# Performance work log

Measured on AMD Instinct MI355X. Metric: run time of the kernel, lower is better.

Reference implementation:

```python
import jax, jax.numpy as jnp
import numpy as np
from functools import partial

N_NODES = 100000
N_EDGES = 3200000
F_IN, H1, H2, C_OUT = 128, 64, 32, 2


def setup_inputs() -> dict:
    key = jax.random.key(0)
    ks = jax.random.split(key, 8)
    x = jax.random.normal(ks[0], (N_NODES, F_IN), dtype=jnp.float32)
    edge_index = jax.random.randint(ks[1], (2, N_EDGES), 0, N_NODES, dtype=jnp.int64)
    def glorot(k, fan_in, fan_out):
        s = jnp.sqrt(6.0 / (fan_in + fan_out))
        return jax.random.uniform(k, (fan_in, fan_out), jnp.float32, -s, s)
    return {
        "x": x,
        "edge_index": edge_index,
        "W1": glorot(ks[2], F_IN, H1), "b1": jnp.zeros((H1,), jnp.float32),
        "W2": glorot(ks[3], H1, H2),   "b2": jnp.zeros((H2,), jnp.float32),
        "W3": glorot(ks[4], H2, C_OUT), "b3": jnp.zeros((C_OUT,), jnp.float32),
    }


def _gcn_norm(edge_index, num_nodes):
    # add self-loops, compute symmetric normalization D^{-1/2} (A+I) D^{-1/2}
    loop = jnp.arange(num_nodes, dtype=edge_index.dtype)
    src = jnp.concatenate([edge_index[0], loop])
    dst = jnp.concatenate([edge_index[1], loop])
    deg = jax.ops.segment_sum(jnp.ones_like(dst, dtype=jnp.float32), dst,
                              num_segments=num_nodes)
    dinv = jax.lax.rsqrt(deg)  # deg >= 1 because of self-loops
    norm = dinv[src] * dinv[dst]  # [E + N]
    return src, dst, norm


def _gcn_conv(x, W, b, src, dst, norm, num_nodes):
    # PyG GCNConv: linear transform, then normalized scatter-aggregate, then bias
    xw = x @ W                                   # [N, F_out]
    msg = xw[src] * norm[:, None]                # [E+N, F_out] gather + scale
    out = jax.ops.segment_sum(msg, dst, num_segments=num_nodes)
    return out + b


def reference(x, edge_index, W1, b1, W2, b2, W3, b3):
    n = x.shape[0]
    src, dst, norm = _gcn_norm(edge_index, n)
    h = jax.nn.relu(_gcn_conv(x, W1, b1, src, dst, norm, n))
    # dropout is identity in eval mode
    h = jax.nn.relu(_gcn_conv(h, W2, b2, src, dst, norm, n))
    h = _gcn_conv(h, W3, b3, src, dst, norm, n)
    return jax.nn.log_softmax(h, axis=1)
```

## Files before the change

### kernel.cpp

```cpp
#include <hip/hip_runtime.h>
#include <hip/hip_bf16.h>
#include <math.h>

constexpr int N = 100000;
constexpr int E = 3200000;
constexpr int FIN = 128, H1 = 64, H2 = 32, COUT = 2;

constexpr int BUK_SHIFT = 6;
constexpr int BUK_NODES = 64;
constexpr int NBUK = (N + BUK_NODES - 1) / BUK_NODES;
constexpr int CAP = 2560;
constexpr int SEG_SHIFT = 14;
constexpr int NSEG = 7;
constexpr int KEYS = BUK_NODES * NSEG;
constexpr int RP_STR = BUK_NODES + 1;

constexpr int MS_TPB = 1024;
constexpr int MS_EPT = 24;
constexpr int CHUNK = MS_TPB * MS_EPT;
constexpr int MS_WGS = (E + CHUNK - 1) / CHUNK;

typedef float f32x4 __attribute__((ext_vector_type(4)));
typedef short bf16x8 __attribute__((ext_vector_type(8)));
typedef short s16x4 __attribute__((ext_vector_type(4)));

__global__ void k_initcur(int* __restrict__ gcursor) {
    int i = blockIdx.x * blockDim.x + threadIdx.x;
    if (i < NBUK) gcursor[i] = i * CAP;
}

__global__ __launch_bounds__(MS_TPB)
void k_mslice(const int* __restrict__ src, const int* __restrict__ dst,
              int* __restrict__ gcursor, unsigned* __restrict__ ebuf) {
    __shared__ int cnt[NBUK];
    __shared__ int base[NBUK];
    const int t = threadIdx.x;
    for (int i = t; i < NBUK; i += MS_TPB) cnt[i] = 0;
    __syncthreads();
    const int e0 = blockIdx.x * CHUNK;

    int rb[MS_EPT];
    unsigned rv[MS_EPT];
#pragma unroll
    for (int j = 0; j < MS_EPT; ++j) {
        int e = e0 + j * MS_TPB + t;
        if (e < E) {
            int d = dst[e];
            int b = d >> BUK_SHIFT;
            rb[j] = b;
            rv[j] = (unsigned)src[e] | ((unsigned)(d & (BUK_NODES - 1)) << 17);
            atomicAdd(&cnt[b], 1);
        } else {
            rb[j] = -1; rv[j] = 0;
        }
    }
    __syncthreads();
    for (int i = t; i < NBUK; i += MS_TPB) {
        int c = cnt[i];
        base[i] = c ? atomicAdd(&gcursor[i], c) : 0;
    }
    __syncthreads();
    for (int i = t; i < NBUK; i += MS_TPB) cnt[i] = 0;
    __syncthreads();
#pragma unroll
    for (int j = 0; j < MS_EPT; ++j) {
        int b = rb[j];
        if (b >= 0) {
            int r = atomicAdd(&cnt[b], 1);
            int p = base[b] + r;
            if (p < (b + 1) * CAP) ebuf[p] = rv[j];
        }
    }
}

__global__ __launch_bounds__(256)
void k_build(const int* __restrict__ gcursor, unsigned* __restrict__ ebuf,
             int* __restrict__ rp, float* __restrict__ dinv) {
    __shared__ unsigned ent[CAP];
    __shared__ int cnt[512];
    __shared__ int sa[512];
    __shared__ int sb[512];
    __shared__ int cur[512];
    const int b = blockIdx.x;
    const int t = threadIdx.x;
    int fill = gcursor[b] - b * CAP;
    if (fill > CAP) fill = CAP;
    const int gbase = b * CAP;

    cnt[t] = 0; cnt[t + 256] = 0;
    __syncthreads();
    for (int j = t; j < fill; j += 256) {
        unsigned v = ebuf[gbase + j];
        ent[j] = v;
        int key = (int)(v >> 17) * NSEG + (int)((v & 0x1FFFFu) >> SEG_SHIFT);
        atomicAdd(&cnt[key], 1);
    }
    __syncthreads();
    sa[t] = cnt[t]; sa[t + 256] = cnt[t + 256];
    __syncthreads();
    int* pin = sa; int* pout = sb;
    for (int off = 1; off < 512; off <<= 1) {
        pout[t]       = pin[t]       + ((t >= off)       ? pin[t - off]       : 0);
        pout[t + 256] = pin[t + 256] + ((t + 256 >= off) ? pin[t + 256 - off] : 0);
        __syncthreads();
        int* tmp = pin; pin = pout; pout = tmp;
    }
    {
        int ex0 = pin[t] - cnt[t];
        int ex1 = pin[t + 256] - cnt[t + 256];
        cur[t] = gbase + ex0;
        cur[t + 256] = gbase + ex1;
        if (t < KEYS && (t % NSEG) == 0)
            rp[b * RP_STR + t / NSEG] = gbase + ex0;
        int k2 = t + 256;
        if (k2 < KEYS && (k2 % NSEG) == 0)
            rp[b * RP_STR + k2 / NSEG] = gbase + ex1;
        if (t == 0) rp[b * RP_STR + BUK_NODES] = gbase + fill;
    }
    if (t < BUK_NODES) {
        int deg = 0;
#pragma unroll
        for (int s = 0; s < NSEG; ++s) deg += cnt[t * NSEG + s];
        int node = (b << BUK_SHIFT) + t;
        if (node < N) dinv[node] = rsqrtf((float)deg + 1.0f);
    }
    __syncthreads();
    for (int j = t; j < fill; j += 256) {
        unsigned v = ent[j];
        int key = (int)(v >> 17) * NSEG + (int)((v & 0x1FFFFu) >> SEG_SHIFT);
        int p = atomicAdd(&cur[key], 1);
        ebuf[p] = v & 0x1FFFFu;
    }
}

template<int FI, int FO>
__global__ __launch_bounds__(256)
void k_gemm_mfma(const float* __restrict__ h, const float* __restrict__ Wg,
                 const float* __restrict__ dinv, __hip_bfloat16* __restrict__ y) {
    constexpr int KH  = (FI > 64) ? 64 : FI;
    constexpr int NPH = FI / KH;
    constexpr int KP  = KH + 8;
    constexpr int NCT = FO / 16;

    __shared__ short xh[64 * KP];
    __shared__ short xl[64 * KP];
    __shared__ short wh[FO * KP];
    __shared__ short wl[FO * KP];

    const int tid = threadIdx.x;
    const int w   = tid >> 6;
    const int l   = tid & 63;
    const int lm  = l & 15;
    const int lg  = l >> 4;
    const int row0 = blockIdx.x * 64;

    auto cvt_hi = [](float f) -> short {
        __hip_bfloat16 b = __float2bfloat16(f);
        return *reinterpret_cast<short*>(&b);
    };
    auto bf2f = [](short s) -> float {
        return __uint_as_float(((unsigned)(unsigned short)s) << 16);
    };

    f32x4 acc[NCT];
#pragma unroll
    for (int ct = 0; ct < NCT; ++ct) acc[ct] = f32x4{0.f, 0.f, 0.f, 0.f};

    for (int ph = 0; ph < NPH; ++ph) {
        if (ph) __syncthreads();
        for (int idx = tid; idx < 64 * KH / 4; idx += 256) {
            int r  = idx / (KH / 4);
            int k4 = idx % (KH / 4);
            int row = row0 + r;
            float4 v = make_float4(0.f, 0.f, 0.f, 0.f);
            if (row < N) v = *(const float4*)(h + (size_t)row * FI + ph * KH + 4 * k4);
            float vv[4] = {v.x, v.y, v.z, v.w};
            s16x4 ph4, pl4;
#pragma unroll
            for (int i = 0; i < 4; ++i) {
                short hi = cvt_hi(vv[i]);
                ph4[i] = hi;
                pl4[i] = cvt_hi(vv[i] - bf2f(hi));
            }
            *(s16x4*)&xh[r * KP + 4 * k4] = ph4;
            *(s16x4*)&xl[r * KP + 4 * k4] = pl4;
        }
        for (int idx = tid; idx < KH * FO; idx += 256) {
            int k = idx / FO;
            int c = idx % FO;
            float wv = Wg[(size_t)(ph * KH + k) * FO + c];
            short hi = cvt_hi(wv);
            wh[c * KP + k] = hi;
            wl[c * KP + k] = cvt_hi(wv - bf2f(hi));
        }
        __syncthreads();

#pragma unroll
        for (int k0 = 0; k0 < KH; k0 += 32) {
            const int ka = (16 * w + lm) * KP + k0 + 8 * lg;
            bf16x8 ah = *(const bf16x8*)&xh[ka];
            bf16x8 al = *(const bf16x8*)&xl[ka];
#pragma unroll
            for (int ct = 0; ct < NCT; ++ct) {
                const int kb = (16 * ct + lm) * KP + k0 + 8 * lg;
                bf16x8 bh = *(const bf16x8*)&wh[kb];
                bf16x8 bl = *(const bf16x8*)&wl[kb];
                acc[ct] = __builtin_amdgcn_mfma_f32_16x16x32_bf16(ah, bh, acc[ct], 0, 0, 0);
                acc[ct] = __builtin_amdgcn_mfma_f32_16x16x32_bf16(ah, bl, acc[ct], 0, 0, 0);
                acc[ct] = __builtin_amdgcn_mfma_f32_16x16x32_bf16(al, bh, acc[ct], 0, 0, 0);
            }
        }
    }

    float di[4];
#pragma unroll
    for (int i = 0; i < 4; ++i) {
        int row = row0 + 16 * w + 4 * lg + i;
        di[i] = (row < N) ? dinv[row] : 0.f;
    }
#pragma unroll
    for (int ct = 0; ct < NCT; ++ct) {
#pragma unroll
        for (int i = 0; i < 4; ++i) {
            int row = row0 + 16 * w + 4 * lg + i;
            if (row < N)
                y[(size_t)row * FO + 16 * ct + lm] = __float2bfloat16(di[i] * acc[ct][i]);
        }
    }
}

template<int FI, int FO, int ROWS>
__global__ __launch_bounds__(FO * ROWS)
void k_gemm_scale(const float* __restrict__ h, const float* __restrict__ W,
                  const float* __restrict__ dinv, float* __restrict__ y) {
    __shared__ float xs[ROWS][FI];
    const int j = threadIdx.x;
    const int r = threadIdx.y;
    const int row0 = blockIdx.x * ROWS;
    const int tid = r * FO + j;
    constexpr int NT = FO * ROWS;
    for (int t = tid; t < ROWS * FI; t += NT) {
        int rr = t / FI, kk = t % FI;
        int row = row0 + rr;
        xs[rr][kk] = (row < N) ? h[(size_t)row * FI + kk] : 0.0f;
    }
    __syncthreads();
    const int row = row0 + r;
    if (row >= N) return;
    float acc = 0.0f;
#pragma unroll
    for (int k = 0; k < FI; ++k)
        acc = fmaf(xs[r][k], W[k * FO + j], acc);
    y[(size_t)row * FO + j] = dinv[row] * acc;
}

template<int F, bool RELU>
__global__ __launch_bounds__(256)
void k_agg_v(const int* __restrict__ rp, const unsigned* __restrict__ csr,
             const __hip_bfloat16* __restrict__ y, const float* __restrict__ dinv,
             const float* __restrict__ b, float* __restrict__ out) {
    constexpr int LPN = F / 8;
    constexpr int NPB = 256 / LPN;
    const int fp = threadIdx.x;
    const int n = blockIdx.x * NPB + threadIdx.y;
    if (n >= N) return;
    const uint4* yq = (const uint4*)y;

    float acc[8];
    auto unpk = [](unsigned w, float& lo, float& hi) {
        lo = __uint_as_float(w << 16);
        hi = __uint_as_float(w & 0xffff0000u);
    };
    auto accum = [&](uint4 v) {
        float l0, h0, l1, h1, l2, h2, l3, h3;
        unpk(v.x, l0, h0); unpk(v.y, l1, h1);
        unpk(v.z, l2, h2); unpk(v.w, l3, h3);
        acc[0] += l0; acc[1] += h0; acc[2] += l1; acc[3] += h1;
        acc[4] += l2; acc[5] += h2; acc[6] += l3; acc[7] += h3;
    };

    {
        uint4 v = yq[(size_t)n * LPN + fp];
        float l0, h0, l1, h1, l2, h2, l3, h3;
        unpk(v.x, l0, h0); unpk(v.y, l1, h1);
        unpk(v.z, l2, h2); unpk(v.w, l3, h3);
        acc[0] = l0; acc[1] = h0; acc[2] = l1; acc[3] = h1;
        acc[4] = l2; acc[5] = h2; acc[6] = l3; acc[7] = h3;
    }

    const int rb = (n >> BUK_SHIFT) * RP_STR + (n & (BUK_NODES - 1));
    int j = rp[rb];
    const int j1 = rp[rb + 1];
    for (; j + 8 <= j1; j += 8) {
        int s0 = (int)csr[j],     s1 = (int)csr[j + 1], s2 = (int)csr[j + 2], s3 = (int)csr[j + 3];
        int s4 = (int)csr[j + 4], s5 = (int)csr[j + 5], s6 = (int)csr[j + 6], s7 = (int)csr[j + 7];
        uint4 v0 = yq[(size_t)s0 * LPN + fp], v1 = yq[(size_t)s1 * LPN + fp];
        uint4 v2 = yq[(size_t)s2 * LPN + fp], v3 = yq[(size_t)s3 * LPN + fp];
        uint4 v4 = yq[(size_t)s4 * LPN + fp], v5 = yq[(size_t)s5 * LPN + fp];
        uint4 v6 = yq[(size_t)s6 * LPN + fp], v7 = yq[(size_t)s7 * LPN + fp];
        accum(v0); accum(v1); accum(v2); accum(v3);
        accum(v4); accum(v5); accum(v6); accum(v7);
    }
    for (; j < j1; ++j) {
        uint4 v = yq[(size_t)(int)csr[j] * LPN + fp];
        accum(v);
    }

    const float di = dinv[n];
    float4 o0, o1;
    o0.x = fmaf(di, acc[0], b[8 * fp + 0]);
    o0.y = fmaf(di, acc[1], b[8 * fp + 1]);
    o0.z = fmaf(di, acc[2], b[8 * fp + 2]);
    o0.w = fmaf(di, acc[3], b[8 * fp + 3]);
    o1.x = fmaf(di, acc[4], b[8 * fp + 4]);
    o1.y = fmaf(di, acc[5], b[8 * fp + 5]);
    o1.z = fmaf(di, acc[6], b[8 * fp + 6]);
    o1.w = fmaf(di, acc[7], b[8 * fp + 7]);
    if (RELU) {
        o0.x = fmaxf(o0.x, 0.f); o0.y = fmaxf(o0.y, 0.f);
        o0.z = fmaxf(o0.z, 0.f); o0.w = fmaxf(o0.w, 0.f);
        o1.x = fmaxf(o1.x, 0.f); o1.y = fmaxf(o1.y, 0.f);
        o1.z = fmaxf(o1.z, 0.f); o1.w = fmaxf(o1.w, 0.f);
    }
    float* op = out + (size_t)n * F + 8 * fp;
    *(float4*)op = o0;
    *(float4*)(op + 4) = o1;
}

__global__ __launch_bounds__(256)
void k_final(const int* __restrict__ rp, const unsigned* __restrict__ csr,
             const float* __restrict__ y, const float* __restrict__ dinv,
             const float* __restrict__ bias, float* __restrict__ out) {
    const int c = threadIdx.x;
    const int n = blockIdx.x * 128 + threadIdx.y;
    float z = 0.0f;
    if (n < N) {
        const int rb = (n >> BUK_SHIFT) * RP_STR + (n & (BUK_NODES - 1));
        int j = rp[rb];
        const int j1 = rp[rb + 1];
        float acc = y[2 * n + c];
        for (; j + 4 <= j1; j += 4) {
            int s0 = (int)csr[j], s1 = (int)csr[j + 1], s2 = (int)csr[j + 2], s3 = (int)csr[j + 3];
            float a0 = y[2 * s0 + c], a1 = y[2 * s1 + c];
            float a2 = y[2 * s2 + c], a3 = y[2 * s3 + c];
            acc += (a0 + a1) + (a2 + a3);
        }
        for (; j < j1; ++j) acc += y[2 * (int)csr[j] + c];
        z = fmaf(dinv[n], acc, bias[c]);
    }
    float zo = __shfl_xor(z, 1);
    if (n < N) {
        float m = fmaxf(z, zo);
        float lse = m + logf(expf(z - m) + expf(zo - m));
        out[2 * n + c] = z - lse;
    }
}

extern "C" void kernel_launch(void* const* d_in, const int* in_sizes, int n_in,
                              void* d_out, int out_size, void* d_ws, size_t ws_size,
                              hipStream_t stream) {
    const float* x   = (const float*)d_in[0];
    const int*   ei  = (const int*)d_in[1];
    const float* W1  = (const float*)d_in[2];
    const float* b1  = (const float*)d_in[3];
    const float* W2  = (const float*)d_in[4];
    const float* b2  = (const float*)d_in[5];
    const float* W3  = (const float*)d_in[6];
    const float* b3  = (const float*)d_in[7];
    float* out = (float*)d_out;

    const int* src = ei;
    const int* dst = ei + E;

    char* p = (char*)d_ws;
    float*    dinv    = (float*)p;    p += (size_t)N * 4;
    int*      gcursor = (int*)p;      p += (size_t)NBUK * 4;
    int*      rp      = (int*)p;      p += (size_t)NBUK * RP_STR * 4;
    unsigned* ebuf    = (unsigned*)p; p += (size_t)NBUK * CAP * 4;
    char*     bufA    = p;            p += (size_t)N * 64 * 4;
    char*     bufB    = p;            p += (size_t)N * 64 * 4;

    __hip_bfloat16* y1 = (__hip_bfloat16*)bufA;
    float*          h1 = (float*)bufB;
    __hip_bfloat16* y2 = (__hip_bfloat16*)bufA;
    float*          h2 = (float*)(bufA + (size_t)N * H2 * 2);
    float*          y3 = (float*)bufB;

    k_initcur<<<(NBUK + 255) / 256, 256, 0, stream>>>(gcursor);
    k_mslice <<<MS_WGS, MS_TPB, 0, stream>>>(src, dst, gcursor, ebuf);
    k_build  <<<NBUK, 256, 0, stream>>>(gcursor, ebuf, rp, dinv);

    k_gemm_mfma<FIN, H1><<<(N + 63) / 64, 256, 0, stream>>>(x, W1, dinv, y1);
    k_agg_v<H1, true><<<(N + 31) / 32, dim3(8, 32), 0, stream>>>(rp, ebuf, y1, dinv, b1, h1);

    k_gemm_mfma<H1, H2><<<(N + 63) / 64, 256, 0, stream>>>(h1, W2, dinv, y2);
    k_agg_v<H2, true><<<(N + 63) / 64, dim3(4, 64), 0, stream>>>(rp, ebuf, y2, dinv, b2, h2);

    k_gemm_scale<H2, COUT, 128><<<(N + 127) / 128, dim3(COUT, 128), 0, stream>>>(h2, W3, dinv, y3);
    k_final<<<(N + 127) / 128, dim3(2, 128), 0, stream>>>(rp, ebuf, y3, dinv, b3, out);
}
```

Baseline: 369.0 us.

## Split feature dim into 16-wide slices for cache-resident neighbor aggregation

The GEMM now writes its bf16 output slice-major ([F/16][N][16]). Aggregation runs as one launch per 16-feature slice, so each pass gathers from a 3.2 MB table that is more likely to stay in L2 or the last-level cache. Index reads and output writes use nontemporal hints so they don't evict the gathered table. In exchange the CSR indices are re-read once per slice, there are more kernel launches, and each gathered row is a 32-byte access instead of a full 128-byte row.

```diff
diff --git a/kernel.cpp b/kernel.cpp
--- a/kernel.cpp
+++ b/kernel.cpp
@@ -224,7 +224,7 @@
         for (int i = 0; i < 4; ++i) {
             int row = row0 + 16 * w + 4 * lg + i;
             if (row < N)
-                y[(size_t)row * FO + 16 * ct + lm] = __float2bfloat16(di[i] * acc[ct][i]);
+                y[((size_t)ct * N + row) * 16 + lm] = __float2bfloat16(di[i] * acc[ct][i]);
         }
     }
 }
@@ -256,21 +256,26 @@
 
 template<int F, bool RELU>
 __global__ __launch_bounds__(256)
-void k_agg_v(const int* __restrict__ rp, const unsigned* __restrict__ csr,
-             const __hip_bfloat16* __restrict__ y, const float* __restrict__ dinv,
-             const float* __restrict__ b, float* __restrict__ out) {
-    constexpr int LPN = F / 8;
-    constexpr int NPB = 256 / LPN;
+void k_agg_slice(int ps, const int* __restrict__ rp, const unsigned* __restrict__ csr,
+                 const __hip_bfloat16* __restrict__ y, const float* __restrict__ dinv,
+                 const float* __restrict__ b, float* __restrict__ out) {
     const int fp = threadIdx.x;
-    const int n = blockIdx.x * NPB + threadIdx.y;
+    const int n  = blockIdx.x * 128 + threadIdx.y;
     if (n >= N) return;
     const uint4* yq = (const uint4*)y;
-
-    float acc[8];
+    const size_t sb = (size_t)ps * N * 2 + fp;
+
     auto unpk = [](unsigned w, float& lo, float& hi) {
         lo = __uint_as_float(w << 16);
         hi = __uint_as_float(w & 0xffff0000u);
     };
+
+    float acc[8];
+    {
+        uint4 v = yq[sb + (size_t)n * 2];
+        unpk(v.x, acc[0], acc[1]); unpk(v.y, acc[2], acc[3]);
+        unpk(v.z, acc[4], acc[5]); unpk(v.w, acc[6], acc[7]);
+    }
     auto accum = [&](uint4 v) {
         float l0, h0, l1, h1, l2, h2, l3, h3;
         unpk(v.x, l0, h0); unpk(v.y, l1, h1);
@@ -279,52 +284,50 @@
         acc[4] += l2; acc[5] += h2; acc[6] += l3; acc[7] += h3;
     };
 
-    {
-        uint4 v = yq[(size_t)n * LPN + fp];
-        float l0, h0, l1, h1, l2, h2, l3, h3;
-        unpk(v.x, l0, h0); unpk(v.y, l1, h1);
-        unpk(v.z, l2, h2); unpk(v.w, l3, h3);
-        acc[0] = l0; acc[1] = h0; acc[2] = l1; acc[3] = h1;
-        acc[4] = l2; acc[5] = h2; acc[6] = l3; acc[7] = h3;
-    }
-
     const int rb = (n >> BUK_SHIFT) * RP_STR + (n & (BUK_NODES - 1));
     int j = rp[rb];
     const int j1 = rp[rb + 1];
     for (; j + 8 <= j1; j += 8) {
-        int s0 = (int)csr[j],     s1 = (int)csr[j + 1], s2 = (int)csr[j + 2], s3 = (int)csr[j + 3];
-        int s4 = (int)csr[j + 4], s5 = (int)csr[j + 5], s6 = (int)csr[j + 6], s7 = (int)csr[j + 7];
-        uint4 v0 = yq[(size_t)s0 * LPN + fp], v1 = yq[(size_t)s1 * LPN + fp];
-        uint4 v2 = yq[(size_t)s2 * LPN + fp], v3 = yq[(size_t)s3 * LPN + fp];
-        uint4 v4 = yq[(size_t)s4 * LPN + fp], v5 = yq[(size_t)s5 * LPN + fp];
-        uint4 v6 = yq[(size_t)s6 * LPN + fp], v7 = yq[(size_t)s7 * LPN + fp];
+        int s0 = (int)__builtin_nontemporal_load(&csr[j]);
+        int s1 = (int)__builtin_nontemporal_load(&csr[j + 1]);
+        int s2 = (int)__builtin_nontemporal_load(&csr[j + 2]);
+        int s3 = (int)__builtin_nontemporal_load(&csr[j + 3]);
+        int s4 = (int)__builtin_nontemporal_load(&csr[j + 4]);
+        int s5 = (int)__builtin_nontemporal_load(&csr[j + 5]);
+        int s6 = (int)__builtin_nontemporal_load(&csr[j + 6]);
+        int s7 = (int)__builtin_nontemporal_load(&csr[j + 7]);
+        uint4 v0 = yq[sb + (size_t)s0 * 2], v1 = yq[sb + (size_t)s1 * 2];
+        uint4 v2 = yq[sb + (size_t)s2 * 2], v3 = yq[sb + (size_t)s3 * 2];
+        uint4 v4 = yq[sb + (size_t)s4 * 2], v5 = yq[sb + (size_t)s5 * 2];
+        uint4 v6 = yq[sb + (size_t)s6 * 2], v7 = yq[sb + (size_t)s7 * 2];
         accum(v0); accum(v1); accum(v2); accum(v3);
         accum(v4); accum(v5); accum(v6); accum(v7);
     }
     for (; j < j1; ++j) {
-        uint4 v = yq[(size_t)(int)csr[j] * LPN + fp];
-        accum(v);
+        int s = (int)__builtin_nontemporal_load(&csr[j]);
+        accum(yq[sb + (size_t)s * 2]);
     }
 
     const float di = dinv[n];
-    float4 o0, o1;
-    o0.x = fmaf(di, acc[0], b[8 * fp + 0]);
-    o0.y = fmaf(di, acc[1], b[8 * fp + 1]);
-    o0.z = fmaf(di, acc[2], b[8 * fp + 2]);
-    o0.w = fmaf(di, acc[3], b[8 * fp + 3]);
-    o1.x = fmaf(di, acc[4], b[8 * fp + 4]);
-    o1.y = fmaf(di, acc[5], b[8 * fp + 5]);
-    o1.z = fmaf(di, acc[6], b[8 * fp + 6]);
-    o1.w = fmaf(di, acc[7], b[8 * fp + 7]);
+    const float* bp = b + ps * 16 + 8 * fp;
+    f32x4 o0, o1;
+    o0.x = fmaf(di, acc[0], bp[0]);
+    o0.y = fmaf(di, acc[1], bp[1]);
+    o0.z = fmaf(di, acc[2], bp[2]);
+    o0.w = fmaf(di, acc[3], bp[3]);
+    o1.x = fmaf(di, acc[4], bp[4]);
+    o1.y = fmaf(di, acc[5], bp[5]);
+    o1.z = fmaf(di, acc[6], bp[6]);
+    o1.w = fmaf(di, acc[7], bp[7]);
     if (RELU) {
         o0.x = fmaxf(o0.x, 0.f); o0.y = fmaxf(o0.y, 0.f);
         o0.z = fmaxf(o0.z, 0.f); o0.w = fmaxf(o0.w, 0.f);
         o1.x = fmaxf(o1.x, 0.f); o1.y = fmaxf(o1.y, 0.f);
         o1.z = fmaxf(o1.z, 0.f); o1.w = fmaxf(o1.w, 0.f);
     }
-    float* op = out + (size_t)n * F + 8 * fp;
-    *(float4*)op = o0;
-    *(float4*)(op + 4) = o1;
+    float* op = out + (size_t)n * F + ps * 16 + 8 * fp;
+    __builtin_nontemporal_store(o0, (f32x4*)op);
+    __builtin_nontemporal_store(o1, (f32x4*)(op + 4));
 }
 
 __global__ __launch_bounds__(256)
@@ -390,11 +393,15 @@
     k_mslice <<<MS_WGS, MS_TPB, 0, stream>>>(src, dst, gcursor, ebuf);
     k_build  <<<NBUK, 256, 0, stream>>>(gcursor, ebuf, rp, dinv);
 
+    const int AGG_GRID = (N + 127) / 128;
+
     k_gemm_mfma<FIN, H1><<<(N + 63) / 64, 256, 0, stream>>>(x, W1, dinv, y1);
-    k_agg_v<H1, true><<<(N + 31) / 32, dim3(8, 32), 0, stream>>>(rp, ebuf, y1, dinv, b1, h1);
+    for (int ps = 0; ps < H1 / 16; ++ps)
+        k_agg_slice<H1, true><<<AGG_GRID, dim3(2, 128), 0, stream>>>(ps, rp, ebuf, y1, dinv, b1, h1);
 
     k_gemm_mfma<H1, H2><<<(N + 63) / 64, 256, 0, stream>>>(h1, W2, dinv, y2);
-    k_agg_v<H2, true><<<(N + 63) / 64, dim3(4, 64), 0, stream>>>(rp, ebuf, y2, dinv, b2, h2);
+    for (int ps = 0; ps < H2 / 16; ++ps)
+        k_agg_slice<H2, true><<<AGG_GRID, dim3(2, 128), 0, stream>>>(ps, rp, ebuf, y2, dinv, b2, h2);
 
     k_gemm_scale<H2, COUT, 128><<<(N + 127) / 128, dim3(COUT, 128), 0, stream>>>(h2, W3, dinv, y3);
     k_final<<<(N + 127) / 128, dim3(2, 128), 0, stream>>>(rp, ebuf, y3, dinv, b3, out);
```

Result: slower. 511.9 us (+38.7%).
